# Performance work log

Measured on AMD Instinct MI355X. Metric: run time of the kernel, lower is better.

Reference implementation:

```python
import jax, jax.numpy as jnp
import numpy as np

N = 30000        # num nodes
R = 16           # num relations
B = 30           # num bases (hard-coded in source)
E = 960000       # num edges (avg degree 32)
IN, HID, OUT, ADR = 128, 128, 64, 400


def setup_inputs() -> dict:
    key = jax.random.key(0)
    ks = jax.random.split(key, 13)
    s_in = 1.0 / np.sqrt(IN)
    s_hid = 1.0 / np.sqrt(HID)
    s_out = 1.0 / np.sqrt(OUT)
    return {
        "x": jax.random.normal(ks[0], (N, IN), jnp.float32),
        "edge_index": jax.random.randint(ks[1], (2, E), 0, N, jnp.int64),
        "edge_type": jax.random.randint(ks[2], (E,), 0, R, jnp.int64),
        "comp1": jax.random.normal(ks[3], (R, B), jnp.float32) * (1.0 / np.sqrt(B)),
        "basis1": jax.random.normal(ks[4], (B, IN, HID), jnp.float32) * s_in,
        "root1": jax.random.normal(ks[5], (IN, HID), jnp.float32) * s_in,
        "bias1": jnp.zeros((HID,), jnp.float32),
        "comp2": jax.random.normal(ks[6], (R, B), jnp.float32) * (1.0 / np.sqrt(B)),
        "basis2": jax.random.normal(ks[7], (B, HID, OUT), jnp.float32) * s_hid,
        "root2": jax.random.normal(ks[8], (HID, OUT), jnp.float32) * s_hid,
        "bias2": jnp.zeros((OUT,), jnp.float32),
        "wc": jax.random.normal(ks[9], (OUT, ADR), jnp.float32) * s_out,
        "bc": jnp.zeros((ADR,), jnp.float32),
    }


def _rgcn_conv(x, src, dst, etype, comp, basis, root, bias):
    """PyG RGCNConv: out[i] = sum_r mean_{e: dst=i, rel=r} x[src_e] @ W_r + x[i] @ root + bias,
    with basis decomposition W_r = sum_b comp[r,b] * basis[b].
    Aggregate-first: segment-mean x[src] into (node, relation) buckets, then contract."""
    n, din = x.shape
    seg = dst * R + etype                                   # [E] composite segment id
    msg = x[src]                                            # [E, din] edge gather
    sums = jax.ops.segment_sum(msg, seg, num_segments=n * R)            # [N*R, din]
    cnt = jax.ops.segment_sum(jnp.ones((src.shape[0],), x.dtype), seg,
                              num_segments=n * R)                       # [N*R]
    mean = sums / jnp.maximum(cnt, 1.0)[:, None]            # per-relation mean
    agg = mean.reshape(n, R, din)                           # [N, R, din]
    w = jnp.einsum('rb,bio->rio', comp, basis)              # [R, din, dout]
    return jnp.einsum('nri,rio->no', agg, w) + x @ root + bias


def reference(x, edge_index, edge_type, comp1, basis1, root1, bias1,
              comp2, basis2, root2, bias2, wc, bc):
    src, dst = edge_index[0], edge_index[1]
    h = _rgcn_conv(x, src, dst, edge_type, comp1, basis1, root1, bias1)
    h = jax.nn.relu(h)
    h = _rgcn_conv(h, src, dst, edge_type, comp2, basis2, root2, bias2)
    return h @ wc + bc
```

## Files before the change

kernel.cpp:

```cpp
#include <hip/hip_runtime.h>

#define R_    16
#define NBAS  30
#define DIN1  128
#define DHID  128
#define DOUT2 64
#define DADR  400
#define KCH   128

typedef __attribute__((ext_vector_type(8))) short bf16x8;
typedef __attribute__((ext_vector_type(4))) float f32x4;

__device__ __forceinline__ short f2bf(float f) {
    unsigned u = __float_as_uint(f);
    u += 0x7fffu + ((u >> 16) & 1u);
    return (short)(u >> 16);
}
__device__ __forceinline__ unsigned packbf(float lo, float hi) {
    return (unsigned)(unsigned short)f2bf(lo) | ((unsigned)(unsigned short)f2bf(hi) << 16);
}

struct Row8 { f32x4 lo, hi; };

__device__ __forceinline__ Row8 row8_zero() {
    Row8 z; z.lo = (f32x4){0.f,0.f,0.f,0.f}; z.hi = (f32x4){0.f,0.f,0.f,0.f}; return z;
}
__device__ __forceinline__ Row8 row8_add(Row8 a, int4 v) {
    unsigned u0 = (unsigned)v.x, u1 = (unsigned)v.y, u2 = (unsigned)v.z, u3 = (unsigned)v.w;
    a.lo[0] += __uint_as_float(u0 << 16);
    a.lo[1] += __uint_as_float(u0 & 0xffff0000u);
    a.lo[2] += __uint_as_float(u1 << 16);
    a.lo[3] += __uint_as_float(u1 & 0xffff0000u);
    a.hi[0] += __uint_as_float(u2 << 16);
    a.hi[1] += __uint_as_float(u2 & 0xffff0000u);
    a.hi[2] += __uint_as_float(u3 << 16);
    a.hi[3] += __uint_as_float(u3 & 0xffff0000u);
    return a;
}
__device__ __forceinline__ int4 row8_pack(Row8 a) {
    int4 o;
    o.x = (int)packbf(a.lo[0], a.lo[1]);
    o.y = (int)packbf(a.lo[2], a.lo[3]);
    o.z = (int)packbf(a.hi[0], a.hi[1]);
    o.w = (int)packbf(a.hi[2], a.hi[3]);
    return o;
}

__device__ __forceinline__ void gload_lds16(const void* g, void* l) {
    __builtin_amdgcn_global_load_lds(
        (const __attribute__((address_space(1))) unsigned int*)g,
        (__attribute__((address_space(3))) unsigned int*)l, 16, 0, 0);
}

__device__ __forceinline__ size_t swzidx(int r, int o, int k, int chStride) {
    int ib = ((o * 256 + ((k >> 3) << 4)) ^ ((o & 15) << 4)) + ((k & 7) << 1);
    return (size_t)r * chStride + (ib >> 1);
}

__device__ __forceinline__ Row8 gather_idx(const short* __restrict__ featbf,
                                           const int* __restrict__ srt,
                                           int b, int c, int idx, int l16) {
    Row8 a = row8_zero();
    int s = c < 16 ? c : 16;
    int j = 0;
    for (; j + 4 <= s; j += 4) {
        int i0 = __shfl(idx, j, 16);
        int i1 = __shfl(idx, j + 1, 16);
        int i2 = __shfl(idx, j + 2, 16);
        int i3 = __shfl(idx, j + 3, 16);
        int4 v0 = *(const int4*)(featbf + (size_t)i0 * KCH + l16 * 8);
        int4 v1 = *(const int4*)(featbf + (size_t)i1 * KCH + l16 * 8);
        int4 v2 = *(const int4*)(featbf + (size_t)i2 * KCH + l16 * 8);
        int4 v3 = *(const int4*)(featbf + (size_t)i3 * KCH + l16 * 8);
        a = row8_add(a, v0); a = row8_add(a, v1);
        a = row8_add(a, v2); a = row8_add(a, v3);
    }
    for (; j + 2 <= s; j += 2) {
        int i0 = __shfl(idx, j, 16);
        int i1 = __shfl(idx, j + 1, 16);
        int4 v0 = *(const int4*)(featbf + (size_t)i0 * KCH + l16 * 8);
        int4 v1 = *(const int4*)(featbf + (size_t)i1 * KCH + l16 * 8);
        a = row8_add(a, v0); a = row8_add(a, v1);
    }
    if (j < s) {
        int i0 = __shfl(idx, j, 16);
        a = row8_add(a, *(const int4*)(featbf + (size_t)i0 * KCH + l16 * 8));
    }
    for (int p = b + 16; p < b + c; ++p)
        a = row8_add(a, *(const int4*)(featbf + (size_t)srt[p] * KCH + l16 * 8));
    float sc = 1.f / (float)(c > 1 ? c : 1);
    a.lo *= sc; a.hi *= sc;
    return a;
}

#define PREP1 (R_ * DIN1 * DHID)
#define PREP2 (PREP1 + R_ * DHID * DOUT2)
#define PREP3 (PREP2 + DIN1 * DHID)
#define PREP4 (PREP3 + DHID * DOUT2)
#define PREP5 (PREP4 + DADR * DOUT2)
__global__ __launch_bounds__(256)
void setup_kernel(const float* __restrict__ x, short* __restrict__ xbf, int n4,
                  const int* __restrict__ dst, const int* __restrict__ ety,
                  int* __restrict__ cnt, int E, int N,
                  const float* __restrict__ comp1, const float* __restrict__ basis1,
                  const float* __restrict__ root1,
                  const float* __restrict__ comp2, const float* __restrict__ basis2,
                  const float* __restrict__ root2,
                  const float* __restrict__ wc,
                  short* __restrict__ BT1, short* __restrict__ BT2,
                  short* __restrict__ wcT) {
    int gid = blockIdx.x * 256 + threadIdx.x;
    if (gid < n4) {
        float4 v = ((const float4*)x)[gid];
        short4 b = { f2bf(v.x), f2bf(v.y), f2bf(v.z), f2bf(v.w) };
        ((short4*)xbf)[gid] = b;
        return;
    }
    gid -= n4;
    if (gid < E) {
        atomicAdd(&cnt[ety[gid] * N + dst[gid]], 1);
        return;
    }
    int idx = gid - E;
    if (idx < PREP1) {
        int o = idx % DHID, i = (idx / DHID) % DIN1, r = idx / (DHID * DIN1);
        float acc = 0.f;
        #pragma unroll 6
        for (int b = 0; b < NBAS; ++b)
            acc += comp1[r * NBAS + b] * basis1[((size_t)b * DIN1 + i) * DHID + o];
        BT1[swzidx(r, o, i, DHID * 128)] = f2bf(acc);
    } else if (idx < PREP2) {
        int t = idx - PREP1;
        int o = t % DOUT2, i = (t / DOUT2) % DHID, r = t / (DOUT2 * DHID);
        float acc = 0.f;
        #pragma unroll 6
        for (int b = 0; b < NBAS; ++b)
            acc += comp2[r * NBAS + b] * basis2[((size_t)b * DHID + i) * DOUT2 + o];
        BT2[swzidx(r, o, i, DOUT2 * 128)] = f2bf(acc);
    } else if (idx < PREP3) {
        int t = idx - PREP2;
        int o = t % DHID, i = t / DHID;
        BT1[swzidx(R_, o, i, DHID * 128)] = f2bf(root1[(size_t)i * DHID + o]);
    } else if (idx < PREP4) {
        int t = idx - PREP3;
        int o = t % DOUT2, i = t / DOUT2;
        BT2[swzidx(R_, o, i, DOUT2 * 128)] = f2bf(root2[(size_t)i * DOUT2 + o]);
    } else if (idx < PREP5) {
        int t = idx - PREP4;
        int a = t / DOUT2, k = t % DOUT2;
        wcT[(size_t)a * DOUT2 + k] = f2bf(wc[(size_t)k * DADR + a]);
    }
}

#define SCAN_CHUNK 2048
#define SCAN_IT    8

__global__ __launch_bounds__(256) void scan_bsum_kernel(const int* __restrict__ cnt, int nseg,
                                                        int* __restrict__ bsum) {
    __shared__ int sd[256];
    int base = blockIdx.x * SCAN_CHUNK;
    int s = 0;
    #pragma unroll
    for (int j = 0; j < SCAN_IT; ++j) {
        int idx = base + j * 256 + threadIdx.x;
        if (idx < nseg) s += cnt[idx];
    }
    sd[threadIdx.x] = s;
    __syncthreads();
    for (int st = 128; st > 0; st >>= 1) {
        if (threadIdx.x < st) sd[threadIdx.x] += sd[threadIdx.x + st];
        __syncthreads();
    }
    if (threadIdx.x == 0) bsum[blockIdx.x] = sd[0];
}

__global__ __launch_bounds__(256) void scan_top_kernel(const int* __restrict__ bsum, int nblk,
                                                       int* __restrict__ boff,
                                                       int* __restrict__ off, int nseg) {
    if (nblk > 256) {
        if (threadIdx.x == 0) {
            int run = 0;
            for (int i = 0; i < nblk; ++i) { int t = bsum[i]; boff[i] = run; run += t; }
            off[nseg] = run;
        }
        return;
    }
    __shared__ int sd[256];
    int v = (threadIdx.x < nblk) ? bsum[threadIdx.x] : 0;
    sd[threadIdx.x] = v;
    __syncthreads();
    for (int st = 1; st < 256; st <<= 1) {
        int t = (threadIdx.x >= st) ? sd[threadIdx.x - st] : 0;
        __syncthreads();
        sd[threadIdx.x] += t;
        __syncthreads();
    }
    if (threadIdx.x < nblk) boff[threadIdx.x] = sd[threadIdx.x] - v;
    if (threadIdx.x == nblk - 1) off[nseg] = sd[threadIdx.x];
}

__global__ __launch_bounds__(256) void scan_final_kernel(const int* __restrict__ cnt, int nseg,
                                                         const int* __restrict__ boff,
                                                         int* __restrict__ off,
                                                         int* __restrict__ cursor) {
    __shared__ int sd[256];
    int base = blockIdx.x * SCAN_CHUNK + threadIdx.x * SCAN_IT;
    int v[SCAN_IT];
    int s = 0;
    #pragma unroll
    for (int j = 0; j < SCAN_IT; ++j) {
        int idx = base + j;
        v[j] = (idx < nseg) ? cnt[idx] : 0;
        s += v[j];
    }
    sd[threadIdx.x] = s;
    __syncthreads();
    for (int st = 1; st < 256; st <<= 1) {
        int t = (threadIdx.x >= st) ? sd[threadIdx.x - st] : 0;
        __syncthreads();
        sd[threadIdx.x] += t;
        __syncthreads();
    }
    int run = boff[blockIdx.x] + sd[threadIdx.x] - s;
    #pragma unroll
    for (int j = 0; j < SCAN_IT; ++j) {
        int idx = base + j;
        if (idx < nseg) { off[idx] = run; cursor[idx] = run; }
        run += v[j];
    }
}

__global__ __launch_bounds__(256) void reorder_kernel(const int* __restrict__ src,
                                                      const int* __restrict__ dst,
                                                      const int* __restrict__ ety,
                                                      int* __restrict__ cursor,
                                                      int* __restrict__ srt, int E, int N) {
    int e = blockIdx.x * blockDim.x + threadIdx.x;
    if (e >= E) return;
    int seg = ety[e] * N + dst[e];
    int pos = atomicAdd(&cursor[seg], 1);
    srt[pos] = src[e];
}

template<int BN, bool OUTBF>
__global__ __launch_bounds__(256, 4)
void rgcn_fused_kernel(const short* __restrict__ featbf,
                       const int* __restrict__ off2,
                       const int* __restrict__ srt,
                       const short* __restrict__ BT,
                       const float* __restrict__ bias,
                       void* __restrict__ Hout, int N, int relu)
{
    constexpr int BM = 32, BK = 128;
    constexpr int WN = BN / 4;
    constexpr int MR = 2;
    constexpr int NR = WN / 16;
    constexpr int NCOPY = BN / 16;

    __shared__ short lA[BM * BK];
    __shared__ short lB[BN * BK];

    const int tid  = threadIdx.x;
    const int lane = tid & 63;
    const int wv   = tid >> 6;
    const int g16  = tid >> 4;
    const int l16  = tid & 15;
    const int n0   = blockIdx.x * BM;
    const int row0 = n0 + g16;
    const int row1 = n0 + 16 + g16;

    f32x4 acc[MR][NR];
    #pragma unroll
    for (int m = 0; m < MR; ++m)
        #pragma unroll
        for (int n = 0; n < NR; ++n)
            acc[m][n] = (f32x4){0.f, 0.f, 0.f, 0.f};

    int b0v = 0, e0v = 0, b1v = 0, e1v = 0;
    if (row0 < N) { b0v = off2[l16 * N + row0]; e0v = off2[l16 * N + row0 + 1]; }
    if (row1 < N) { b1v = off2[l16 * N + row1]; e1v = off2[l16 * N + row1 + 1]; }

    int cb0 = __shfl(b0v, 0, 16), cc0 = __shfl(e0v, 0, 16) - cb0;
    int cb1 = __shfl(b1v, 0, 16), cc1 = __shfl(e1v, 0, 16) - cb1;
    int cidx0 = (l16 < (cc0 < 16 ? cc0 : 16)) ? srt[cb0 + l16] : 0;
    int cidx1 = (l16 < (cc1 < 16 ? cc1 : 16)) ? srt[cb1 + l16] : 0;

    for (int r = 0; r <= R_; ++r) {
        __syncthreads();

        {
            const char* srcB = (const char*)BT + (size_t)r * BN * 256;
            #pragma unroll
            for (int j = 0; j < NCOPY; ++j) {
                const char* g = srcB + j * 4096 + wv * 1024 + (lane << 4);
                char* l = (char*)lB + j * 4096 + wv * 1024;
                gload_lds16(g, l);
            }
        }

        int nb0 = 0, nc0 = 0, nb1 = 0, nc1 = 0, nidx0 = 0, nidx1 = 0;
        if (r + 1 < R_) {
            nb0 = __shfl(b0v, r + 1, 16); nc0 = __shfl(e0v, r + 1, 16) - nb0;
            nb1 = __shfl(b1v, r + 1, 16); nc1 = __shfl(e1v, r + 1, 16) - nb1;
            nidx0 = (l16 < (nc0 < 16 ? nc0 : 16)) ? srt[nb0 + l16] : 0;
            nidx1 = (l16 < (nc1 < 16 ? nc1 : 16)) ? srt[nb1 + l16] : 0;
        }

        Row8 a0, a1;
        if (r < R_) {
            a0 = gather_idx(featbf, srt, cb0, cc0, cidx0, l16);
            a1 = gather_idx(featbf, srt, cb1, cc1, cidx1, l16);
        } else {
            a0 = row8_zero(); a1 = row8_zero();
            if (row0 < N)
                a0 = row8_add(a0, *(const int4*)(featbf + (size_t)row0 * KCH + l16 * 8));
            if (row1 < N)
                a1 = row8_add(a1, *(const int4*)(featbf + (size_t)row1 * KCH + l16 * 8));
        }

        {
            int byte0 = ((g16 * BK + l16 * 8) << 1) ^ ((g16 & 15) << 4);
            *(int4*)((char*)lA + byte0) = row8_pack(a0);
            int rowl = 16 + g16;
            int byte1 = ((rowl * BK + l16 * 8) << 1) ^ ((rowl & 15) << 4);
            *(int4*)((char*)lA + byte1) = row8_pack(a1);
        }
        __syncthreads();

        #pragma unroll
        for (int kk = 0; kk < BK / 32; ++kk) {
            const int kpos = kk * 32 + (lane >> 4) * 8;
            bf16x8 af[MR], bfr[NR];
            #pragma unroll
            for (int m = 0; m < MR; ++m) {
                int row = m * 16 + (lane & 15);
                af[m] = *(const bf16x8*)((const char*)lA +
                         (((row * BK + kpos) << 1) ^ ((row & 15) << 4)));
            }
            #pragma unroll
            for (int n = 0; n < NR; ++n) {
                int col = wv * WN + n * 16 + (lane & 15);
                bfr[n] = *(const bf16x8*)((const char*)lB +
                         (((col * BK + kpos) << 1) ^ ((col & 15) << 4)));
            }
            #pragma unroll
            for (int m = 0; m < MR; ++m)
                #pragma unroll
                for (int n = 0; n < NR; ++n)
                    acc[m][n] = __builtin_amdgcn_mfma_f32_16x16x32_bf16(
                        af[m], bfr[n], acc[m][n], 0, 0, 0);
        }

        cb0 = nb0; cc0 = nc0; cidx0 = nidx0;
        cb1 = nb1; cc1 = nc1; cidx1 = nidx1;
    }

    #pragma unroll
    for (int m = 0; m < MR; ++m)
        #pragma unroll
        for (int n = 0; n < NR; ++n)
            #pragma unroll
            for (int i = 0; i < 4; ++i) {
                int row  = m * 16 + ((lane >> 4) << 2) + i;
                int col  = wv * WN + n * 16 + (lane & 15);
                int grow = n0 + row;
                if (grow >= N) continue;
                float v = acc[m][n][i] + bias[col];
                if (relu) v = fmaxf(v, 0.f);
                if (OUTBF) ((short*)Hout)[(size_t)grow * BN + col] = f2bf(v);
                else       ((float*)Hout)[(size_t)grow * BN + col] = v;
            }
}

__global__ __launch_bounds__(256)
void classifier_gemm_kernel(const short* __restrict__ h2bf,
                            const short* __restrict__ wcT,
                            const float* __restrict__ bc,
                            float* __restrict__ out, int N)
{
    constexpr int BM = 128, BN = 80, BK = 64;
    constexpr int MR = 2, NR = 5;

    __shared__ short lA[BM * BK];
    __shared__ short lB[BN * BK];

    const int tid  = threadIdx.x;
    const int lane = tid & 63;
    const int wv   = tid >> 6;
    const int nodeBase = blockIdx.x * BM;
    const int colBase  = blockIdx.y * BN;

    const int t8  = tid & 7;
    const int r32 = tid >> 3;

    #pragma unroll
    for (int it = 0; it < 4; ++it) {
        int row  = it * 32 + r32;
        int grow = nodeBase + row;
        int4 v = {0, 0, 0, 0};
        if (grow < N) v = *(const int4*)(h2bf + (size_t)grow * DOUT2 + t8 * 8);
        int byte = ((row * BK + t8 * 8) << 1) ^ ((row & 7) << 4);
        *(int4*)((char*)lA + byte) = v;
    }
    for (int o = r32; o < BN; o += 32) {
        int4 v = *(const int4*)(wcT + (size_t)(colBase + o) * DOUT2 + t8 * 8);
        int byte = ((o * BK + t8 * 8) << 1) ^ ((o & 7) << 4);
        *(int4*)((char*)lB + byte) = v;
    }
    __syncthreads();

    f32x4 acc[MR][NR];
    #pragma unroll
    for (int m = 0; m < MR; ++m)
        #pragma unroll
        for (int n = 0; n < NR; ++n)
            acc[m][n] = (f32x4){0.f, 0.f, 0.f, 0.f};

    #pragma unroll
    for (int kk = 0; kk < BK / 32; ++kk) {
        const int kpos = kk * 32 + (lane >> 4) * 8;
        bf16x8 af[MR], bfr[NR];
        #pragma unroll
        for (int m = 0; m < MR; ++m) {
            int row = wv * 32 + m * 16 + (lane & 15);
            af[m] = *(const bf16x8*)((const char*)lA +
                     (((row * BK + kpos) << 1) ^ ((row & 7) << 4)));
        }
        #pragma unroll
        for (int n = 0; n < NR; ++n) {
            int col = n * 16 + (lane & 15);
            bfr[n] = *(const bf16x8*)((const char*)lB +
                     (((col * BK + kpos) << 1) ^ ((col & 7) << 4)));
        }
        #pragma unroll
        for (int m = 0; m < MR; ++m)
            #pragma unroll
            for (int n = 0; n < NR; ++n)
                acc[m][n] = __builtin_amdgcn_mfma_f32_16x16x32_bf16(
                    af[m], bfr[n], acc[m][n], 0, 0, 0);
    }

    #pragma unroll
    for (int m = 0; m < MR; ++m)
        #pragma unroll
        for (int n = 0; n < NR; ++n)
            #pragma unroll
            for (int i = 0; i < 4; ++i) {
                int row  = wv * 32 + m * 16 + ((lane >> 4) << 2) + i;
                int col  = n * 16 + (lane & 15);
                int grow = nodeBase + row;
                if (grow >= N) continue;
                int gcol = colBase + col;
                out[(size_t)grow * DADR + gcol] = acc[m][n][i] + bc[gcol];
            }
}

static inline size_t align16(size_t x) { return (x + 15) & ~(size_t)15; }

extern "C" void kernel_launch(void* const* d_in, const int* in_sizes, int n_in,
                              void* d_out, int out_size, void* d_ws, size_t ws_size,
                              hipStream_t stream) {
    const float* x      = (const float*)d_in[0];
    const int*   ei     = (const int*)d_in[1];
    const int*   et     = (const int*)d_in[2];
    const float* comp1  = (const float*)d_in[3];
    const float* basis1 = (const float*)d_in[4];
    const float* root1  = (const float*)d_in[5];
    const float* bias1  = (const float*)d_in[6];
    const float* comp2  = (const float*)d_in[7];
    const float* basis2 = (const float*)d_in[8];
    const float* root2  = (const float*)d_in[9];
    const float* bias2  = (const float*)d_in[10];
    const float* wc     = (const float*)d_in[11];
    const float* bc     = (const float*)d_in[12];
    float* out = (float*)d_out;

    const int E = in_sizes[1] / 2;
    const int N = in_sizes[0] / DIN1;
    const int* srcp = ei;
    const int* dstp = ei + E;

    const int NSEG = N * R_;
    const int NBLK = (NSEG + SCAN_CHUNK - 1) / SCAN_CHUNK;

    char* ws = (char*)d_ws;
    size_t o = 0;
    int*   cntI   = (int*)(ws + o);   o = align16(o + (size_t)NSEG * 4);
    int*   off2   = (int*)(ws + o);   o = align16(o + (size_t)(NSEG + 1) * 4);
    int*   cursor = (int*)(ws + o);   o = align16(o + (size_t)NSEG * 4);
    int*   bsum   = (int*)(ws + o);   o = align16(o + (size_t)NBLK * 4);
    int*   boff   = (int*)(ws + o);   o = align16(o + (size_t)NBLK * 4);
    int*   srt    = (int*)(ws + o);   o = align16(o + (size_t)E * 4);
    short* BT1    = (short*)(ws + o); o = align16(o + (size_t)(R_ + 1) * DHID * 128 * 2);
    short* BT2    = (short*)(ws + o); o = align16(o + (size_t)(R_ + 1) * DOUT2 * 128 * 2);
    short* wcTb   = (short*)(ws + o); o = align16(o + (size_t)DADR * DOUT2 * 2);
    short* xbf    = (short*)(ws + o); o = align16(o + (size_t)N * DIN1 * 2);
    short* h1bf   = (short*)(ws + o); o = align16(o + (size_t)N * DHID * 2);
    short* h2bf   = (short*)(ws + o); o = align16(o + (size_t)N * DOUT2 * 2);

    const int n4 = N * DIN1 / 4;
    hipMemsetAsync(cntI, 0, (size_t)NSEG * 4, stream);
    {
        long long total = (long long)n4 + E + PREP5;
        int grid = (int)((total + 255) / 256);
        setup_kernel<<<grid, 256, 0, stream>>>(x, xbf, n4, dstp, et, cntI, E, N,
                                               comp1, basis1, root1,
                                               comp2, basis2, root2, wc,
                                               BT1, BT2, wcTb);
    }

    scan_bsum_kernel<<<NBLK, 256, 0, stream>>>(cntI, NSEG, bsum);
    scan_top_kernel<<<1, 256, 0, stream>>>(bsum, NBLK, boff, off2, NSEG);
    scan_final_kernel<<<NBLK, 256, 0, stream>>>(cntI, NSEG, boff, off2, cursor);
    reorder_kernel<<<(E + 255) / 256, 256, 0, stream>>>(srcp, dstp, et, cursor, srt, E, N);

    const int gGrid = (N + 31) / 32;
    rgcn_fused_kernel<DHID, true><<<gGrid, 256, 0, stream>>>(xbf,  off2, srt, BT1, bias1, h1bf, N, 1);
    rgcn_fused_kernel<DOUT2, true><<<gGrid, 256, 0, stream>>>(h1bf, off2, srt, BT2, bias2, h2bf, N, 0);

    dim3 cGrid((N + 127) / 128, DADR / 80);
    classifier_gemm_kernel<<<cGrid, 256, 0, stream>>>(h2bf, wcTb, bc, out, N);
}
```

Measured before the change: 295.3 us.

## Split fused RGCN K dimension into 64-wide chunks across 34 iterations

Restructures the fused gather+MFMA kernel to process the 128-wide feature dimension in two 64-wide halves. It now runs 34 chunk iterations (17 relations/root times 2 halves) instead of 17, and the weight layout and swizzle are rewritten to match. LDS use per block is halved, which may allow more resident blocks and gives more pipelined steps. In exchange, each edge's neighbor indices are re-gathered twice with 8-byte loads instead of once with 16-byte loads, and the number of block barriers doubles.

```diff
diff --git a/kernel.cpp b/kernel.cpp
--- a/kernel.cpp
+++ b/kernel.cpp
@@ -7,6 +7,7 @@
 #define DOUT2 64
 #define DADR  400
 #define KCH   128
+#define NCHUNK 34
 
 typedef __attribute__((ext_vector_type(8))) short bf16x8;
 typedef __attribute__((ext_vector_type(4))) float f32x4;
@@ -20,29 +21,18 @@
     return (unsigned)(unsigned short)f2bf(lo) | ((unsigned)(unsigned short)f2bf(hi) << 16);
 }
 
-struct Row8 { f32x4 lo, hi; };
-
-__device__ __forceinline__ Row8 row8_zero() {
-    Row8 z; z.lo = (f32x4){0.f,0.f,0.f,0.f}; z.hi = (f32x4){0.f,0.f,0.f,0.f}; return z;
-}
-__device__ __forceinline__ Row8 row8_add(Row8 a, int4 v) {
-    unsigned u0 = (unsigned)v.x, u1 = (unsigned)v.y, u2 = (unsigned)v.z, u3 = (unsigned)v.w;
-    a.lo[0] += __uint_as_float(u0 << 16);
-    a.lo[1] += __uint_as_float(u0 & 0xffff0000u);
-    a.lo[2] += __uint_as_float(u1 << 16);
-    a.lo[3] += __uint_as_float(u1 & 0xffff0000u);
-    a.hi[0] += __uint_as_float(u2 << 16);
-    a.hi[1] += __uint_as_float(u2 & 0xffff0000u);
-    a.hi[2] += __uint_as_float(u3 << 16);
-    a.hi[3] += __uint_as_float(u3 & 0xffff0000u);
+__device__ __forceinline__ f32x4 r4_add(f32x4 a, int2 v) {
+    unsigned u0 = (unsigned)v.x, u1 = (unsigned)v.y;
+    a[0] += __uint_as_float(u0 << 16);
+    a[1] += __uint_as_float(u0 & 0xffff0000u);
+    a[2] += __uint_as_float(u1 << 16);
+    a[3] += __uint_as_float(u1 & 0xffff0000u);
     return a;
 }
-__device__ __forceinline__ int4 row8_pack(Row8 a) {
-    int4 o;
-    o.x = (int)packbf(a.lo[0], a.lo[1]);
-    o.y = (int)packbf(a.lo[2], a.lo[3]);
-    o.z = (int)packbf(a.hi[0], a.hi[1]);
-    o.w = (int)packbf(a.hi[2], a.hi[3]);
+__device__ __forceinline__ int2 r4_pack(f32x4 a) {
+    int2 o;
+    o.x = (int)packbf(a[0], a[1]);
+    o.y = (int)packbf(a[2], a[3]);
     return o;
 }
 
@@ -52,15 +42,15 @@
         (__attribute__((address_space(3))) unsigned int*)l, 16, 0, 0);
 }
 
-__device__ __forceinline__ size_t swzidx(int r, int o, int k, int chStride) {
-    int ib = ((o * 256 + ((k >> 3) << 4)) ^ ((o & 15) << 4)) + ((k & 7) << 1);
-    return (size_t)r * chStride + (ib >> 1);
-}
-
-__device__ __forceinline__ Row8 gather_idx(const short* __restrict__ featbf,
-                                           const int* __restrict__ srt,
-                                           int b, int c, int idx, int l16) {
-    Row8 a = row8_zero();
+__device__ __forceinline__ int swz64(int o, int k) {
+    int ib = ((o * 128 + ((k >> 3) << 4)) ^ ((o & 7) << 4)) + ((k & 7) << 1);
+    return ib >> 1;
+}
+
+__device__ __forceinline__ f32x4 gather4(const short* __restrict__ featbf,
+                                         const int* __restrict__ srt,
+                                         int b, int c, int idx, int l16, int hoff) {
+    f32x4 a = (f32x4){0.f, 0.f, 0.f, 0.f};
     int s = c < 16 ? c : 16;
     int j = 0;
     for (; j + 4 <= s; j += 4) {
@@ -68,28 +58,28 @@
         int i1 = __shfl(idx, j + 1, 16);
         int i2 = __shfl(idx, j + 2, 16);
         int i3 = __shfl(idx, j + 3, 16);
-        int4 v0 = *(const int4*)(featbf + (size_t)i0 * KCH + l16 * 8);
-        int4 v1 = *(const int4*)(featbf + (size_t)i1 * KCH + l16 * 8);
-        int4 v2 = *(const int4*)(featbf + (size_t)i2 * KCH + l16 * 8);
-        int4 v3 = *(const int4*)(featbf + (size_t)i3 * KCH + l16 * 8);
-        a = row8_add(a, v0); a = row8_add(a, v1);
-        a = row8_add(a, v2); a = row8_add(a, v3);
+        int2 v0 = *(const int2*)(featbf + (size_t)i0 * KCH + hoff + l16 * 4);
+        int2 v1 = *(const int2*)(featbf + (size_t)i1 * KCH + hoff + l16 * 4);
+        int2 v2 = *(const int2*)(featbf + (size_t)i2 * KCH + hoff + l16 * 4);
+        int2 v3 = *(const int2*)(featbf + (size_t)i3 * KCH + hoff + l16 * 4);
+        a = r4_add(a, v0); a = r4_add(a, v1);
+        a = r4_add(a, v2); a = r4_add(a, v3);
     }
     for (; j + 2 <= s; j += 2) {
         int i0 = __shfl(idx, j, 16);
         int i1 = __shfl(idx, j + 1, 16);
-        int4 v0 = *(const int4*)(featbf + (size_t)i0 * KCH + l16 * 8);
-        int4 v1 = *(const int4*)(featbf + (size_t)i1 * KCH + l16 * 8);
-        a = row8_add(a, v0); a = row8_add(a, v1);
+        int2 v0 = *(const int2*)(featbf + (size_t)i0 * KCH + hoff + l16 * 4);
+        int2 v1 = *(const int2*)(featbf + (size_t)i1 * KCH + hoff + l16 * 4);
+        a = r4_add(a, v0); a = r4_add(a, v1);
     }
     if (j < s) {
         int i0 = __shfl(idx, j, 16);
-        a = row8_add(a, *(const int4*)(featbf + (size_t)i0 * KCH + l16 * 8));
+        a = r4_add(a, *(const int2*)(featbf + (size_t)i0 * KCH + hoff + l16 * 4));
     }
     for (int p = b + 16; p < b + c; ++p)
-        a = row8_add(a, *(const int4*)(featbf + (size_t)srt[p] * KCH + l16 * 8));
+        a = r4_add(a, *(const int2*)(featbf + (size_t)srt[p] * KCH + hoff + l16 * 4));
     float sc = 1.f / (float)(c > 1 ? c : 1);
-    a.lo *= sc; a.hi *= sc;
+    a[0] *= sc; a[1] *= sc; a[2] *= sc; a[3] *= sc;
     return a;
 }
 
@@ -128,7 +118,8 @@
         #pragma unroll 6
         for (int b = 0; b < NBAS; ++b)
             acc += comp1[r * NBAS + b] * basis1[((size_t)b * DIN1 + i) * DHID + o];
-        BT1[swzidx(r, o, i, DHID * 128)] = f2bf(acc);
+        int c = (i >> 6) * 17 + r;
+        BT1[(size_t)c * (DHID * 64) + swz64(o, i & 63)] = f2bf(acc);
     } else if (idx < PREP2) {
         int t = idx - PREP1;
         int o = t % DOUT2, i = (t / DOUT2) % DHID, r = t / (DOUT2 * DHID);
@@ -136,15 +127,18 @@
         #pragma unroll 6
         for (int b = 0; b < NBAS; ++b)
             acc += comp2[r * NBAS + b] * basis2[((size_t)b * DHID + i) * DOUT2 + o];
-        BT2[swzidx(r, o, i, DOUT2 * 128)] = f2bf(acc);
+        int c = (i >> 6) * 17 + r;
+        BT2[(size_t)c * (DOUT2 * 64) + swz64(o, i & 63)] = f2bf(acc);
     } else if (idx < PREP3) {
         int t = idx - PREP2;
         int o = t % DHID, i = t / DHID;
-        BT1[swzidx(R_, o, i, DHID * 128)] = f2bf(root1[(size_t)i * DHID + o]);
+        int c = (i >> 6) * 17 + R_;
+        BT1[(size_t)c * (DHID * 64) + swz64(o, i & 63)] = f2bf(root1[(size_t)i * DHID + o]);
     } else if (idx < PREP4) {
         int t = idx - PREP3;
         int o = t % DOUT2, i = t / DOUT2;
-        BT2[swzidx(R_, o, i, DOUT2 * 128)] = f2bf(root2[(size_t)i * DOUT2 + o]);
+        int c = (i >> 6) * 17 + R_;
+        BT2[(size_t)c * (DOUT2 * 64) + swz64(o, i & 63)] = f2bf(root2[(size_t)i * DOUT2 + o]);
     } else if (idx < PREP5) {
         int t = idx - PREP4;
         int a = t / DOUT2, k = t % DOUT2;
@@ -251,14 +245,14 @@
                        const float* __restrict__ bias,
                        void* __restrict__ Hout, int N, int relu)
 {
-    constexpr int BM = 32, BK = 128;
+    constexpr int BM = 32;
     constexpr int WN = BN / 4;
     constexpr int MR = 2;
     constexpr int NR = WN / 16;
-    constexpr int NCOPY = BN / 16;
-
-    __shared__ short lA[BM * BK];
-    __shared__ short lB[BN * BK];
+    constexpr int NCOPY = BN / 32;
+
+    __shared__ short lA[BM * 64];
+    __shared__ short lB[BN * 64];
 
     const int tid  = threadIdx.x;
     const int lane = tid & 63;
@@ -285,11 +279,11 @@
     int cidx0 = (l16 < (cc0 < 16 ? cc0 : 16)) ? srt[cb0 + l16] : 0;
     int cidx1 = (l16 < (cc1 < 16 ? cc1 : 16)) ? srt[cb1 + l16] : 0;
 
-    for (int r = 0; r <= R_; ++r) {
+    for (int t = 0; t < NCHUNK; ++t) {
         __syncthreads();
 
         {
-            const char* srcB = (const char*)BT + (size_t)r * BN * 256;
+            const char* srcB = (const char*)BT + (size_t)t * BN * 128;
             #pragma unroll
             for (int j = 0; j < NCOPY; ++j) {
                 const char* g = srcB + j * 4096 + wv * 1024 + (lane << 4);
@@ -298,50 +292,48 @@
             }
         }
 
-        int nb0 = 0, nc0 = 0, nb1 = 0, nc1 = 0, nidx0 = 0, nidx1 = 0;
-        if (r + 1 < R_) {
-            nb0 = __shfl(b0v, r + 1, 16); nc0 = __shfl(e0v, r + 1, 16) - nb0;
-            nb1 = __shfl(b1v, r + 1, 16); nc1 = __shfl(e1v, r + 1, 16) - nb1;
-            nidx0 = (l16 < (nc0 < 16 ? nc0 : 16)) ? srt[nb0 + l16] : 0;
-            nidx1 = (l16 < (nc1 < 16 ? nc1 : 16)) ? srt[nb1 + l16] : 0;
-        }
-
-        Row8 a0, a1;
-        if (r < R_) {
-            a0 = gather_idx(featbf, srt, cb0, cc0, cidx0, l16);
-            a1 = gather_idx(featbf, srt, cb1, cc1, cidx1, l16);
-        } else {
-            a0 = row8_zero(); a1 = row8_zero();
-            if (row0 < N)
-                a0 = row8_add(a0, *(const int4*)(featbf + (size_t)row0 * KCH + l16 * 8));
-            if (row1 < N)
-                a1 = row8_add(a1, *(const int4*)(featbf + (size_t)row1 * KCH + l16 * 8));
-        }
+        int nb0 = 0, nc0 = 0, nidx0 = 0, nb1 = 0, nc1 = 0, nidx1 = 0;
+        if (t + 1 < NCHUNK) {
+            int rn = (t + 1) % 17;
+            if (rn < R_) {
+                nb0 = __shfl(b0v, rn, 16); nc0 = __shfl(e0v, rn, 16) - nb0;
+                nb1 = __shfl(b1v, rn, 16); nc1 = __shfl(e1v, rn, 16) - nb1;
+                nidx0 = (l16 < (nc0 < 16 ? nc0 : 16)) ? srt[nb0 + l16] : 0;
+                nidx1 = (l16 < (nc1 < 16 ? nc1 : 16)) ? srt[nb1 + l16] : 0;
+            } else {
+                nc0 = (row0 < N) ? 1 : 0; nidx0 = (row0 < N) ? row0 : 0;
+                nc1 = (row1 < N) ? 1 : 0; nidx1 = (row1 < N) ? row1 : 0;
+            }
+        }
+
+        const int hoff = (t < 17) ? 0 : 64;
+        f32x4 a0 = gather4(featbf, srt, cb0, cc0, cidx0, l16, hoff);
+        f32x4 a1 = gather4(featbf, srt, cb1, cc1, cidx1, l16, hoff);
 
         {
-            int byte0 = ((g16 * BK + l16 * 8) << 1) ^ ((g16 & 15) << 4);
-            *(int4*)((char*)lA + byte0) = row8_pack(a0);
+            int byte0 = (g16 * 128 + (((l16 >> 1) << 4) ^ ((g16 & 7) << 4))) + ((l16 & 1) << 3);
+            *(int2*)((char*)lA + byte0) = r4_pack(a0);
             int rowl = 16 + g16;
-            int byte1 = ((rowl * BK + l16 * 8) << 1) ^ ((rowl & 15) << 4);
-            *(int4*)((char*)lA + byte1) = row8_pack(a1);
-        }
-        __syncthreads();
-
-        #pragma unroll
-        for (int kk = 0; kk < BK / 32; ++kk) {
-            const int kpos = kk * 32 + (lane >> 4) * 8;
+            int byte1 = (rowl * 128 + (((l16 >> 1) << 4) ^ ((rowl & 7) << 4))) + ((l16 & 1) << 3);
+            *(int2*)((char*)lA + byte1) = r4_pack(a1);
+        }
+        __syncthreads();
+
+        #pragma unroll
+        for (int kk = 0; kk < 2; ++kk) {
+            const int u = kk * 4 + (lane >> 4);
             bf16x8 af[MR], bfr[NR];
             #pragma unroll
             for (int m = 0; m < MR; ++m) {
                 int row = m * 16 + (lane & 15);
                 af[m] = *(const bf16x8*)((const char*)lA +
-                         (((row * BK + kpos) << 1) ^ ((row & 15) << 4)));
+                         row * 128 + ((u << 4) ^ ((row & 7) << 4)));
             }
             #pragma unroll
             for (int n = 0; n < NR; ++n) {
                 int col = wv * WN + n * 16 + (lane & 15);
                 bfr[n] = *(const bf16x8*)((const char*)lB +
-                         (((col * BK + kpos) << 1) ^ ((col & 15) << 4)));
+                         col * 128 + ((u << 4) ^ ((col & 7) << 4)));
             }
             #pragma unroll
             for (int m = 0; m < MR; ++m)
@@ -491,8 +483,8 @@
     int*   bsum   = (int*)(ws + o);   o = align16(o + (size_t)NBLK * 4);
     int*   boff   = (int*)(ws + o);   o = align16(o + (size_t)NBLK * 4);
     int*   srt    = (int*)(ws + o);   o = align16(o + (size_t)E * 4);
-    short* BT1    = (short*)(ws + o); o = align16(o + (size_t)(R_ + 1) * DHID * 128 * 2);
-    short* BT2    = (short*)(ws + o); o = align16(o + (size_t)(R_ + 1) * DOUT2 * 128 * 2);
+    short* BT1    = (short*)(ws + o); o = align16(o + (size_t)NCHUNK * DHID * 64 * 2);
+    short* BT2    = (short*)(ws + o); o = align16(o + (size_t)NCHUNK * DOUT2 * 64 * 2);
     short* wcTb   = (short*)(ws + o); o = align16(o + (size_t)DADR * DOUT2 * 2);
     short* xbf    = (short*)(ws + o); o = align16(o + (size_t)N * DIN1 * 2);
     short* h1bf   = (short*)(ws + o); o = align16(o + (size_t)N * DHID * 2);
```

New measurement: 388.9 us. 31.7% more time.
